# Kernel tuning notes

Measured on AMD Instinct MI355X. Metric: run time of the kernel, lower is better.

Reference implementation:

```python
import jax, jax.numpy as jnp
import numpy as np

ALPHA = 0.2
TAU = 1.0  # max(tau_init, 1e-6)
K_CAP = 256 - 1  # cluster_size_max - 1
SCORE_DIM = 256
PROJ = 64
TH_HIDDEN = 128
THETA_IN = 512


def setup_inputs() -> dict:
    key = jax.random.key(0)
    ks = jax.random.split(key, 12)
    B, N, D = 4, 4096, SCORE_DIM
    x = jax.random.normal(ks[0], (B, N, D), dtype=jnp.float32)
    # sparse-ish binary adjacency, stored dense (as the torch module densifies it)
    adj = (jax.random.uniform(ks[1], (B, N, N)) < 0.005).astype(jnp.float32)
    seed_ctx_feats = jax.random.normal(ks[2], (B, 384), dtype=jnp.float32)
    local_stats = jax.random.normal(ks[3], (B, 128), dtype=jnp.float32)
    cluster_mask = (jax.random.uniform(ks[4], (B, N)) < 0.01).astype(jnp.float32)
    cand_mask = (jax.random.uniform(ks[5], (B, N)) < 0.5).astype(jnp.float32)
    s = 1.0 / np.sqrt(D)
    Wq = jax.random.normal(ks[6], (D, PROJ), dtype=jnp.float32) * s
    Wk = jax.random.normal(ks[7], (D, PROJ), dtype=jnp.float32) * s
    th_w1 = jax.random.normal(ks[8], (THETA_IN, TH_HIDDEN), dtype=jnp.float32) * (1.0 / np.sqrt(THETA_IN))
    th_b1 = jnp.zeros((TH_HIDDEN,), dtype=jnp.float32)
    th_w2 = jax.random.normal(ks[9], (TH_HIDDEN, 1), dtype=jnp.float32) * (1.0 / np.sqrt(TH_HIDDEN))
    th_b2 = jnp.zeros((1,), dtype=jnp.float32)
    return {"x": x, "adj": adj, "seed_ctx_feats": seed_ctx_feats,
            "local_stats": local_stats, "cluster_mask": cluster_mask,
            "cand_mask": cand_mask, "Wq": Wq, "Wk": Wk,
            "th_w1": th_w1, "th_b1": th_b1, "th_w2": th_w2, "th_b2": th_b2}


def reference(x, adj, seed_ctx_feats, local_stats, cluster_mask, cand_mask,
              Wq, Wk, th_w1, th_b1, th_w2, th_b2):
    B, N, D = x.shape
    x_k = x @ Wk  # [B, N, 64]
    # seed_repr is None -> take seed node from argmax of cluster_mask
    seed_idx = jnp.argmax(cluster_mask, axis=-1)            # [B]
    q = x[jnp.arange(B), seed_idx] @ Wq                      # [B, 64]
    scores = jnp.einsum('bnp,bp->bn', x_k, q) / jnp.sqrt(jnp.float32(PROJ))
    # edges-to-cluster count and degree (dense adjacency matvec / row-sum)
    e2c = jnp.einsum('bnm,bm->bn', adj, cluster_mask)        # [B, N]
    deg = jnp.maximum(adj.sum(axis=-1), 1.0)                 # [B, N]
    cand_scores = scores + ALPHA * (e2c / deg)
    # threshold head MLP
    theta_in = jnp.concatenate([seed_ctx_feats, local_stats], axis=-1)  # [B, 512]
    h = jax.nn.relu(theta_in @ th_w1 + th_b1)
    theta = (h @ th_w2 + th_b2)[:, 0]                        # [B]
    logits = (cand_scores - theta[:, None]) / TAU
    p = jax.nn.sigmoid(logits) * cand_mask                   # [B, N]
    # soft cap: if more than K_CAP nodes exceed 0.5, keep only top-K_CAP probs
    over = jax.lax.stop_gradient((p > 0.5).astype(p.dtype).sum(axis=-1) - K_CAP)
    need_trim = over > 0                                     # [B]
    _, topk_idx = jax.lax.top_k(p, K_CAP)                    # [B, K_CAP]
    keep = jnp.zeros_like(p).at[jnp.arange(B)[:, None], topk_idx].set(1.0)
    p = jnp.where(need_trim[:, None], p * keep, p)
    # straight-through hard gate
    hard = (p > 0.5).astype(p.dtype) + p - jax.lax.stop_gradient(p)
    expected_size = jax.lax.stop_gradient(p.sum(axis=-1))
    mean_p = jax.lax.stop_gradient(p.mean(axis=-1))
    return hard, p, theta, expected_size, mean_p
```

## Files before the change

### kernel.cpp

```cpp
#include <hip/hip_runtime.h>
#include <math.h>

#define B 4
#define N 4096
#define D 256
#define PROJ 64
#define TH_HIDDEN 128
#define K_CAP 255
#define ALPHA 0.2f
#define ROWS_PER_BLOCK 8
#define BLOCKS_PER_BATCH (N / ROWS_PER_BLOCK)

typedef float floatx4 __attribute__((ext_vector_type(4)));


__global__ __launch_bounds__(256) void score_kernel(
    const float* __restrict__ x, const float* __restrict__ adj,
    const float* __restrict__ cluster_mask, const float* __restrict__ cand_mask,
    const float* __restrict__ seed_ctx, const float* __restrict__ local_stats,
    const float* __restrict__ Wq, const float* __restrict__ Wk,
    const float* __restrict__ th_w1, const float* __restrict__ th_b1,
    const float* __restrict__ th_w2, const float* __restrict__ th_b2,
    float* __restrict__ p_ws, float* __restrict__ theta_out)
{
    const int b = blockIdx.x / BLOCKS_PER_BATCH;
    const int chunk = blockIdx.x % BLOCKS_PER_BATCH;
    const int t = threadIdx.x;
    const int wave = t >> 6;
    const int lane = t & 63;

    __shared__ float s_mask[N];
    __shared__ float s_v[D];
    __shared__ float s_xh[256];
    __shared__ float s_mlp[256];
    __shared__ float s_r[PROJ];
    __shared__ float s_argv[4];
    __shared__ int   s_argi[4];
    __shared__ float s_theta;

    for (int i = t * 4; i < N; i += 1024)
        *(float4*)&s_mask[i] = *(const float4*)&cluster_mask[b * N + i];
    __syncthreads();

    {
        float bestv = -1e30f; int besti = 0;
        for (int i = t; i < N; i += 256) {
            float vv = s_mask[i];
            if (vv > bestv) { bestv = vv; besti = i; }
        }
        for (int off = 32; off; off >>= 1) {
            float v2 = __shfl_down(bestv, off, 64);
            int   i2 = __shfl_down(besti, off, 64);
            if (v2 > bestv || (v2 == bestv && i2 < besti)) { bestv = v2; besti = i2; }
        }
        if (lane == 0) { s_argv[wave] = bestv; s_argi[wave] = besti; }
    }
    __syncthreads();
    if (t == 0) {
        float bv = s_argv[0]; int bi = s_argi[0];
        #pragma unroll
        for (int w = 1; w < 4; ++w) {
            float v2 = s_argv[w]; int i2 = s_argi[w];
            if (v2 > bv || (v2 == bv && i2 < bi)) { bv = v2; bi = i2; }
        }
        s_argi[0] = bi;
    }
    __syncthreads();
    const int seed = s_argi[0];

    s_xh[t] = x[(size_t)b * N * D + (size_t)seed * D + t];
    {
        const int j = t & 127;
        const int h = t >> 7;
        const float* w1 = th_w1 + (size_t)(h * 256) * TH_HIDDEN + j;
        float acc = 0.f;
        if (h == 0) {
            const float* sc = seed_ctx + b * 384;
            #pragma unroll 8
            for (int i = 0; i < 256; ++i) acc += sc[i] * w1[i * TH_HIDDEN];
        } else {
            const float* sc = seed_ctx + b * 384 + 256;
            #pragma unroll 8
            for (int i = 0; i < 128; ++i) acc += sc[i] * w1[i * TH_HIDDEN];
            const float* ls = local_stats + b * 128;
            const float* w1b = w1 + 128 * TH_HIDDEN;
            #pragma unroll 8
            for (int i = 0; i < 128; ++i) acc += ls[i] * w1b[i * TH_HIDDEN];
        }
        s_mlp[t] = acc;
    }
    __syncthreads();

    {
        const int j = (wave << 4) + (lane >> 2);
        const int q = lane & 3;
        const float* xs = s_xh + q * 64;
        const float* wq = Wq + (size_t)(q * 64) * PROJ + j;
        float acc = 0.f;
        #pragma unroll 8
        for (int d = 0; d < 64; ++d) acc += xs[d] * wq[d * PROJ];
        acc += __shfl_xor(acc, 1, 64);
        acc += __shfl_xor(acc, 2, 64);
        if (q == 0) s_r[j] = acc;
    }
    __syncthreads();

    if (t < TH_HIDDEN)
        s_xh[t] = fmaxf(s_mlp[t] + s_mlp[t + 128] + th_b1[t], 0.f);
    __syncthreads();

    {
        const float4* wk = (const float4*)(Wk + (size_t)t * PROJ);
        float acc = 0.f;
        #pragma unroll
        for (int j4 = 0; j4 < PROJ / 4; ++j4) {
            float4 w = wk[j4];
            float4 r4 = *(const float4*)&s_r[j4 * 4];
            acc += w.x * r4.x + w.y * r4.y + w.z * r4.z + w.w * r4.w;
        }
        s_v[t] = acc * 0.125f;
    }
    if (wave == 1) {
        float a2 = s_xh[lane] * th_w2[lane] + s_xh[lane + 64] * th_w2[lane + 64];
        for (int off = 32; off; off >>= 1) a2 += __shfl_down(a2, off, 64);
        if (lane == 0) s_theta = a2 + th_b2[0];
    }
    __syncthreads();

    if (chunk == 0 && t == 0) theta_out[b] = s_theta;

    const float theta = s_theta;
    const int row0 = chunk * ROWS_PER_BLOCK;

    const int n0 = row0 + wave;
    const int n1 = n0 + 4;
    const float* arow0 = adj + (size_t)b * N * N + (size_t)n0 * N;
    const float* arow1 = adj + (size_t)b * N * N + (size_t)n1 * N;

    float deg0 = 0.f, e2c0 = 0.f, deg1 = 0.f, e2c1 = 0.f;
    #pragma unroll
    for (int k = 0; k < N / 256; ++k) {
        const int i = lane * 4 + k * 256;
        floatx4 a0 = __builtin_nontemporal_load((const floatx4*)&arow0[i]);
        floatx4 a1 = __builtin_nontemporal_load((const floatx4*)&arow1[i]);
        float4 m = *(const float4*)&s_mask[i];
        deg0 += a0.x + a0.y + a0.z + a0.w;
        e2c0 += a0.x * m.x + a0.y * m.y + a0.z * m.z + a0.w * m.w;
        deg1 += a1.x + a1.y + a1.z + a1.w;
        e2c1 += a1.x * m.x + a1.y * m.y + a1.z * m.z + a1.w * m.w;
    }
    float sc0, sc1;
    {
        const float* xrow0 = x + (size_t)b * N * D + (size_t)n0 * D;
        const float* xrow1 = x + (size_t)b * N * D + (size_t)n1 * D;
        float4 xv0 = *(const float4*)&xrow0[lane * 4];
        float4 xv1 = *(const float4*)&xrow1[lane * 4];
        float4 vv  = *(const float4*)&s_v[lane * 4];
        sc0 = xv0.x * vv.x + xv0.y * vv.y + xv0.z * vv.z + xv0.w * vv.w;
        sc1 = xv1.x * vv.x + xv1.y * vv.y + xv1.z * vv.z + xv1.w * vv.w;
    }
    for (int off = 32; off > 0; off >>= 1) {
        deg0 += __shfl_down(deg0, off, 64);
        e2c0 += __shfl_down(e2c0, off, 64);
        sc0  += __shfl_down(sc0,  off, 64);
        deg1 += __shfl_down(deg1, off, 64);
        e2c1 += __shfl_down(e2c1, off, 64);
        sc1  += __shfl_down(sc1,  off, 64);
    }
    if (lane == 0) {
        float d0 = fmaxf(deg0, 1.0f);
        float cand0 = sc0 + ALPHA * (e2c0 / d0);
        float p0 = cand_mask[b * N + n0] / (1.f + expf(-(cand0 - theta)));
        p_ws[b * N + n0] = p0;
        float d1 = fmaxf(deg1, 1.0f);
        float cand1 = sc1 + ALPHA * (e2c1 / d1);
        float p1 = cand_mask[b * N + n1] / (1.f + expf(-(cand1 - theta)));
        p_ws[b * N + n1] = p1;
    }
}

__global__ __launch_bounds__(256) void finalize_kernel(float* p_in, float* out)
{
    const int b = blockIdx.x;
    const int t = threadIdx.x;
    const int wave = t >> 6;
    const int lane = t & 63;
    __shared__ float        sp[N];
    __shared__ unsigned int hist[256];
    __shared__ unsigned int s_ured[4];
    __shared__ float        s_wred[4];
    __shared__ unsigned int s_bcast[2];

    for (int i = t * 4; i < N; i += 1024)
        *(float4*)&sp[i] = *(const float4*)&p_in[b * N + i];
    __syncthreads();

    {
        unsigned int c = 0;
        for (int i = t; i < N; i += 256) c += (sp[i] > 0.5f) ? 1u : 0u;
        for (int off = 32; off; off >>= 1) c += __shfl_down(c, off, 64);
        if (lane == 0) s_ured[wave] = c;
    }
    __syncthreads();
    const unsigned int over_cnt = s_ured[0] + s_ured[1] + s_ured[2] + s_ured[3];
    const bool need_trim = over_cnt > K_CAP;
    __syncthreads();

    unsigned int prefix = 0u;
    unsigned int k_rem = K_CAP;
    if (need_trim) {
        for (int pass = 0; pass < 4; ++pass) {
            const int shift = 24 - pass * 8;
            const unsigned int himask = (pass == 0) ? 0u : (0xFFFFFFFFu << (shift + 8));
            hist[t] = 0u;
            __syncthreads();
            for (int i = t; i < N; i += 256) {
                unsigned int u = __float_as_uint(sp[i]);
                if ((u & himask) == prefix)
                    atomicAdd(&hist[(u >> shift) & 255u], 1u);
            }
            __syncthreads();
            if (wave == 0) {
                const unsigned int h0 = hist[lane * 4 + 0];
                const unsigned int h1 = hist[lane * 4 + 1];
                const unsigned int h2 = hist[lane * 4 + 2];
                const unsigned int h3 = hist[lane * 4 + 3];
                const unsigned int s3 = h3, s2 = h2 + s3, s1 = h1 + s2, s0 = h0 + s1;
                unsigned int incl = s0;
                for (int off = 1; off < 64; off <<= 1) {
                    unsigned int o = __shfl_down(incl, off, 64);
                    if (lane + off < 64) incl += o;
                }
                const unsigned int tail = incl - s0;
                const unsigned int gi0 = tail + s0, gi1 = tail + s1,
                                   gi2 = tail + s2, gi3 = tail + s3;
                if (gi0 - h0 < k_rem && k_rem <= gi0) {
                    s_bcast[0] = prefix | ((unsigned int)(lane * 4 + 0) << shift);
                    s_bcast[1] = k_rem - (gi0 - h0);
                }
                if (gi1 - h1 < k_rem && k_rem <= gi1) {
                    s_bcast[0] = prefix | ((unsigned int)(lane * 4 + 1) << shift);
                    s_bcast[1] = k_rem - (gi1 - h1);
                }
                if (gi2 - h2 < k_rem && k_rem <= gi2) {
                    s_bcast[0] = prefix | ((unsigned int)(lane * 4 + 2) << shift);
                    s_bcast[1] = k_rem - (gi2 - h2);
                }
                if (gi3 - h3 < k_rem && k_rem <= gi3) {
                    s_bcast[0] = prefix | ((unsigned int)(lane * 4 + 3) << shift);
                    s_bcast[1] = k_rem - (gi3 - h3);
                }
            }
            __syncthreads();
            prefix = s_bcast[0];
            k_rem  = s_bcast[1];
            __syncthreads();
        }
    }
    const float vk = __uint_as_float(prefix);
    const unsigned int t_keep = k_rem;

    unsigned int tie_excl = 0;
    if (need_trim) {
        unsigned int local_tie = 0;
        const int base = t * 16;
        for (int j = 0; j < 16; ++j)
            local_tie += (__float_as_uint(sp[base + j]) == prefix) ? 1u : 0u;
        unsigned int incl = local_tie;
        for (int off = 1; off < 64; off <<= 1) {
            unsigned int o = __shfl_up(incl, off, 64);
            if (lane >= off) incl += o;
        }
        if (lane == 63) s_ured[wave] = incl;
        __syncthreads();
        unsigned int woff = 0;
        for (int w = 0; w < wave; ++w) woff += s_ured[w];
        tie_excl = woff + incl - local_tie;
    }

    float psum = 0.f;
    {
        const int base = t * 16;
        unsigned int tie_rank = tie_excl;
        for (int j = 0; j < 16; ++j) {
            const int i = base + j;
            float p = sp[i];
            if (need_trim) {
                const unsigned int u = __float_as_uint(p);
                bool keep;
                if (u == prefix) { keep = (tie_rank < t_keep); tie_rank++; }
                else             { keep = (p > vk); }
                if (!keep) p = 0.f;
            }
            out[b * N + i]         = (p > 0.5f) ? 1.0f : 0.0f;
            out[B * N + b * N + i] = p;
            psum += p;
        }
    }
    for (int off = 32; off; off >>= 1) psum += __shfl_down(psum, off, 64);
    if (lane == 0) s_wred[wave] = psum;
    __syncthreads();
    if (t == 0) {
        const float tot = s_wred[0] + s_wred[1] + s_wred[2] + s_wred[3];
        out[2 * B * N + B + b]     = tot;
        out[2 * B * N + 2 * B + b] = tot * (1.0f / N);
    }
}

extern "C" void kernel_launch(void* const* d_in, const int* in_sizes, int n_in,
                              void* d_out, int out_size, void* d_ws, size_t ws_size,
                              hipStream_t stream) {
    const float* x            = (const float*)d_in[0];
    const float* adj          = (const float*)d_in[1];
    const float* seed_ctx     = (const float*)d_in[2];
    const float* local_stats  = (const float*)d_in[3];
    const float* cluster_mask = (const float*)d_in[4];
    const float* cand_mask    = (const float*)d_in[5];
    const float* Wq           = (const float*)d_in[6];
    const float* Wk           = (const float*)d_in[7];
    const float* th_w1        = (const float*)d_in[8];
    const float* th_b1        = (const float*)d_in[9];
    const float* th_w2        = (const float*)d_in[10];
    const float* th_b2        = (const float*)d_in[11];
    float* out = (float*)d_out;

    float* p_ws     = out + B * N;
    float* theta_ws = out + 2 * B * N;

    hipLaunchKernelGGL(score_kernel, dim3(B * BLOCKS_PER_BATCH), dim3(256), 0, stream,
                       x, adj, cluster_mask, cand_mask, seed_ctx, local_stats,
                       Wq, Wk, th_w1, th_b1, th_w2, th_b2, p_ws, theta_ws);
    hipLaunchKernelGGL(finalize_kernel, dim3(B), dim3(256), 0, stream,
                       p_ws, out);
}
```

Baseline: 421.4 us.

## Hoist per-batch seed projection and threshold MLP into a separate prep kernel

Before, each of the 2048 score blocks redundantly ran the argmax, seed projection through Wq and Wk, and the threshold MLP for its batch. That work now runs once per batch in a small prep kernel, which writes v and theta to workspace (v goes into the hard-output region, which finalize later overwrites). Score blocks then only load v and theta before streaming adj. This adds an extra launch and a serial dependency, but removes many redundant weight reads and syncs from the bandwidth-bound main kernel.

After: 391.7 us, median of 2. 7.0% less time.

```diff
diff --git a/kernel.cpp b/kernel.cpp
--- a/kernel.cpp
+++ b/kernel.cpp
@@ -14,14 +14,142 @@
 typedef float floatx4 __attribute__((ext_vector_type(4)));
 
 
-__global__ __launch_bounds__(256) void score_kernel(
-    const float* __restrict__ x, const float* __restrict__ adj,
-    const float* __restrict__ cluster_mask, const float* __restrict__ cand_mask,
+__global__ __launch_bounds__(256) void prep_kernel(
+    const float* __restrict__ x, const float* __restrict__ cluster_mask,
     const float* __restrict__ seed_ctx, const float* __restrict__ local_stats,
     const float* __restrict__ Wq, const float* __restrict__ Wk,
     const float* __restrict__ th_w1, const float* __restrict__ th_b1,
     const float* __restrict__ th_w2, const float* __restrict__ th_b2,
-    float* __restrict__ p_ws, float* __restrict__ theta_out)
+    float* v_ws, float* theta_out)
+{
+    const int bb = blockIdx.x;
+    const int t = threadIdx.x;
+
+    if (bb >= B) {
+        const int b = bb - B;
+        __shared__ float  s_in[512];
+        __shared__ float4 s_p4[8][32];
+        __shared__ float  s_h[TH_HIDDEN];
+
+        if (t < 96)       ((float4*)s_in)[t]      = ((const float4*)(seed_ctx + b * 384))[t];
+        else if (t < 128) ((float4*)s_in)[t]      = ((const float4*)(local_stats + b * 128))[t - 96];
+        __syncthreads();
+
+        {
+            const int g = t & 31;
+            const int k = t >> 5;
+            const float* w1 = th_w1 + (size_t)(k * 64) * TH_HIDDEN + 4 * g;
+            const float* xin = s_in + k * 64;
+            float4 a = {0.f, 0.f, 0.f, 0.f};
+            #pragma unroll 8
+            for (int i = 0; i < 64; ++i) {
+                const float xv = xin[i];
+                const float4 w = *(const float4*)(w1 + (size_t)i * TH_HIDDEN);
+                a.x += xv * w.x; a.y += xv * w.y; a.z += xv * w.z; a.w += xv * w.w;
+            }
+            s_p4[k][g] = a;
+        }
+        __syncthreads();
+        if (t < 32) {
+            float4 s = s_p4[0][t];
+            #pragma unroll
+            for (int kk = 1; kk < 8; ++kk) {
+                const float4 q = s_p4[kk][t];
+                s.x += q.x; s.y += q.y; s.z += q.z; s.w += q.w;
+            }
+            const float4 b1 = *(const float4*)(th_b1 + 4 * t);
+            s_h[4 * t + 0] = fmaxf(s.x + b1.x, 0.f);
+            s_h[4 * t + 1] = fmaxf(s.y + b1.y, 0.f);
+            s_h[4 * t + 2] = fmaxf(s.z + b1.z, 0.f);
+            s_h[4 * t + 3] = fmaxf(s.w + b1.w, 0.f);
+        }
+        __syncthreads();
+        if (t < 64) {
+            float a2 = s_h[t] * th_w2[t] + s_h[t + 64] * th_w2[t + 64];
+            for (int off = 32; off; off >>= 1) a2 += __shfl_down(a2, off, 64);
+            if (t == 0) theta_out[b] = a2 + th_b2[0];
+        }
+        return;
+    }
+
+    const int b = bb;
+    __shared__ float  s_red[256];
+    __shared__ int    s_idx[256];
+    __shared__ float  s_xseed[D];
+    __shared__ float4 s_q4[16][16];
+    __shared__ float  s_r[PROJ];
+
+    float4 wk[16];
+    {
+        const float4* wkp = (const float4*)(Wk + (size_t)t * PROJ);
+        #pragma unroll
+        for (int j = 0; j < 16; ++j) wk[j] = wkp[j];
+    }
+
+    float bestv = -1e30f; int besti = 0;
+    for (int i = t; i < N; i += 256) {
+        float vv = cluster_mask[b * N + i];
+        if (vv > bestv) { bestv = vv; besti = i; }
+    }
+    s_red[t] = bestv; s_idx[t] = besti;
+    __syncthreads();
+    for (int s = 128; s > 0; s >>= 1) {
+        if (t < s) {
+            float v2 = s_red[t + s]; int i2 = s_idx[t + s];
+            if (v2 > s_red[t] || (v2 == s_red[t] && i2 < s_idx[t])) {
+                s_red[t] = v2; s_idx[t] = i2;
+            }
+        }
+        __syncthreads();
+    }
+    const int seed = s_idx[0];
+
+    s_xseed[t] = x[(size_t)b * N * D + (size_t)seed * D + t];
+    __syncthreads();
+
+    {
+        const int g = t & 15;
+        const int k = t >> 4;
+        const float* wq = Wq + (size_t)(k * 16) * PROJ + 4 * g;
+        const float* xs = s_xseed + k * 16;
+        float4 a = {0.f, 0.f, 0.f, 0.f};
+        #pragma unroll
+        for (int i = 0; i < 16; ++i) {
+            const float xv = xs[i];
+            const float4 w = *(const float4*)(wq + (size_t)i * PROJ);
+            a.x += xv * w.x; a.y += xv * w.y; a.z += xv * w.z; a.w += xv * w.w;
+        }
+        s_q4[k][g] = a;
+    }
+    __syncthreads();
+    if (t < 16) {
+        float4 s = s_q4[0][t];
+        #pragma unroll
+        for (int kk = 1; kk < 16; ++kk) {
+            const float4 q = s_q4[kk][t];
+            s.x += q.x; s.y += q.y; s.z += q.z; s.w += q.w;
+        }
+        *(float4*)&s_r[4 * t] = s;
+    }
+    __syncthreads();
+
+    {
+        float acc = 0.f;
+        #pragma unroll
+        for (int j4 = 0; j4 < PROJ / 4; ++j4) {
+            const float4 w = wk[j4];
+            const float4 r4 = *(const float4*)&s_r[j4 * 4];
+            acc += w.x * r4.x + w.y * r4.y + w.z * r4.z + w.w * r4.w;
+        }
+        v_ws[b * D + t] = acc * 0.125f;
+    }
+}
+
+__global__ __launch_bounds__(256) void score_kernel(
+    const float* __restrict__ x, const float* __restrict__ adj,
+    const float* __restrict__ cluster_mask, const float* __restrict__ cand_mask,
+    const float* __restrict__ v_ws, const float* __restrict__ theta_ws,
+    float* __restrict__ p_ws)
 {
     const int b = blockIdx.x / BLOCKS_PER_BATCH;
     const int chunk = blockIdx.x % BLOCKS_PER_BATCH;
@@ -31,105 +159,13 @@
 
     __shared__ float s_mask[N];
     __shared__ float s_v[D];
-    __shared__ float s_xh[256];
-    __shared__ float s_mlp[256];
-    __shared__ float s_r[PROJ];
-    __shared__ float s_argv[4];
-    __shared__ int   s_argi[4];
-    __shared__ float s_theta;
 
     for (int i = t * 4; i < N; i += 1024)
         *(float4*)&s_mask[i] = *(const float4*)&cluster_mask[b * N + i];
-    __syncthreads();
-
-    {
-        float bestv = -1e30f; int besti = 0;
-        for (int i = t; i < N; i += 256) {
-            float vv = s_mask[i];
-            if (vv > bestv) { bestv = vv; besti = i; }
-        }
-        for (int off = 32; off; off >>= 1) {
-            float v2 = __shfl_down(bestv, off, 64);
-            int   i2 = __shfl_down(besti, off, 64);
-            if (v2 > bestv || (v2 == bestv && i2 < besti)) { bestv = v2; besti = i2; }
-        }
-        if (lane == 0) { s_argv[wave] = bestv; s_argi[wave] = besti; }
-    }
-    __syncthreads();
-    if (t == 0) {
-        float bv = s_argv[0]; int bi = s_argi[0];
-        #pragma unroll
-        for (int w = 1; w < 4; ++w) {
-            float v2 = s_argv[w]; int i2 = s_argi[w];
-            if (v2 > bv || (v2 == bv && i2 < bi)) { bv = v2; bi = i2; }
-        }
-        s_argi[0] = bi;
-    }
-    __syncthreads();
-    const int seed = s_argi[0];
-
-    s_xh[t] = x[(size_t)b * N * D + (size_t)seed * D + t];
-    {
-        const int j = t & 127;
-        const int h = t >> 7;
-        const float* w1 = th_w1 + (size_t)(h * 256) * TH_HIDDEN + j;
-        float acc = 0.f;
-        if (h == 0) {
-            const float* sc = seed_ctx + b * 384;
-            #pragma unroll 8
-            for (int i = 0; i < 256; ++i) acc += sc[i] * w1[i * TH_HIDDEN];
-        } else {
-            const float* sc = seed_ctx + b * 384 + 256;
-            #pragma unroll 8
-            for (int i = 0; i < 128; ++i) acc += sc[i] * w1[i * TH_HIDDEN];
-            const float* ls = local_stats + b * 128;
-            const float* w1b = w1 + 128 * TH_HIDDEN;
-            #pragma unroll 8
-            for (int i = 0; i < 128; ++i) acc += ls[i] * w1b[i * TH_HIDDEN];
-        }
-        s_mlp[t] = acc;
-    }
-    __syncthreads();
-
-    {
-        const int j = (wave << 4) + (lane >> 2);
-        const int q = lane & 3;
-        const float* xs = s_xh + q * 64;
-        const float* wq = Wq + (size_t)(q * 64) * PROJ + j;
-        float acc = 0.f;
-        #pragma unroll 8
-        for (int d = 0; d < 64; ++d) acc += xs[d] * wq[d * PROJ];
-        acc += __shfl_xor(acc, 1, 64);
-        acc += __shfl_xor(acc, 2, 64);
-        if (q == 0) s_r[j] = acc;
-    }
-    __syncthreads();
-
-    if (t < TH_HIDDEN)
-        s_xh[t] = fmaxf(s_mlp[t] + s_mlp[t + 128] + th_b1[t], 0.f);
-    __syncthreads();
-
-    {
-        const float4* wk = (const float4*)(Wk + (size_t)t * PROJ);
-        float acc = 0.f;
-        #pragma unroll
-        for (int j4 = 0; j4 < PROJ / 4; ++j4) {
-            float4 w = wk[j4];
-            float4 r4 = *(const float4*)&s_r[j4 * 4];
-            acc += w.x * r4.x + w.y * r4.y + w.z * r4.z + w.w * r4.w;
-        }
-        s_v[t] = acc * 0.125f;
-    }
-    if (wave == 1) {
-        float a2 = s_xh[lane] * th_w2[lane] + s_xh[lane + 64] * th_w2[lane + 64];
-        for (int off = 32; off; off >>= 1) a2 += __shfl_down(a2, off, 64);
-        if (lane == 0) s_theta = a2 + th_b2[0];
-    }
-    __syncthreads();
-
-    if (chunk == 0 && t == 0) theta_out[b] = s_theta;
-
-    const float theta = s_theta;
+    if (t < D) s_v[t] = v_ws[b * D + t];
+    __syncthreads();
+
+    const float theta = theta_ws[b];
     const int row0 = chunk * ROWS_PER_BLOCK;
 
     const int n0 = row0 + wave;
@@ -324,12 +360,15 @@
     const float* th_b2        = (const float*)d_in[11];
     float* out = (float*)d_out;
 
+    float* v_ws     = out;
     float* p_ws     = out + B * N;
     float* theta_ws = out + 2 * B * N;
 
+    hipLaunchKernelGGL(prep_kernel, dim3(2 * B), dim3(256), 0, stream,
+                       x, cluster_mask, seed_ctx, local_stats, Wq, Wk,
+                       th_w1, th_b1, th_w2, th_b2, v_ws, theta_ws);
     hipLaunchKernelGGL(score_kernel, dim3(B * BLOCKS_PER_BATCH), dim3(256), 0, stream,
-                       x, adj, cluster_mask, cand_mask, seed_ctx, local_stats,
-                       Wq, Wk, th_w1, th_b1, th_w2, th_b2, p_ws, theta_ws);
+                       x, adj, cluster_mask, cand_mask, v_ws, theta_ws, p_ws);
     hipLaunchKernelGGL(finalize_kernel, dim3(B), dim3(256), 0, stream,
                        p_ws, out);
 }
```
